# Kernel optimization log

Measured on AMD Instinct MI355X. Metric: run time of the kernel, lower is better.

The kernel has to match this reference:

```python
import jax, jax.numpy as jnp
import numpy as np

EMBED_DIM = 1024
NUM_HEADS = 16
HEAD_DIM = EMBED_DIM // NUM_HEADS


def setup_inputs() -> dict:
    key = jax.random.key(0)
    k1, k2, k3, k4 = jax.random.split(key, 4)
    S, B = 2048, 2
    x = jax.random.normal(k1, (S, B, EMBED_DIM), dtype=jnp.float32)
    # xavier_uniform for in_proj_weight [3E, E]
    limit_in = float(np.sqrt(6.0 / (3 * EMBED_DIM + EMBED_DIM)))
    in_proj_weight = jax.random.uniform(k2, (3 * EMBED_DIM, EMBED_DIM), minval=-limit_in, maxval=limit_in, dtype=jnp.float32)
    in_proj_bias = jnp.zeros((3 * EMBED_DIM,), dtype=jnp.float32)
    # out_proj: nn.Linear default init (kaiming-uniform-ish); use uniform of similar scale
    limit_out = float(np.sqrt(1.0 / EMBED_DIM))
    out_proj_weight = jax.random.uniform(k3, (EMBED_DIM, EMBED_DIM), minval=-limit_out, maxval=limit_out, dtype=jnp.float32)
    out_proj_bias = jnp.zeros((EMBED_DIM,), dtype=jnp.float32)
    return {
        "x": x,
        "in_proj_weight": in_proj_weight,
        "in_proj_bias": in_proj_bias,
        "out_proj_weight": out_proj_weight,
        "out_proj_bias": out_proj_bias,
    }


def reference(x, in_proj_weight, in_proj_bias, out_proj_weight, out_proj_bias):
    S, B, E = x.shape
    H, D = NUM_HEADS, HEAD_DIM
    scaling = float(D) ** -0.5
    # fused QKV projection: [S, B, 3E]
    qkv = jnp.einsum("sbe,fe->sbf", x, in_proj_weight) + in_proj_bias
    q, k, v = jnp.split(qkv, 3, axis=-1)
    q = q * scaling
    # [S, B, E] -> [B*H, S, D]
    def to_heads(t):
        return t.reshape(S, B * H, D).transpose(1, 0, 2)
    q, k, v = to_heads(q), to_heads(k), to_heads(v)
    # attention scores [B*H, S, S]
    scores = jnp.einsum("btd,bsd->bts", q, k)
    weights = jax.nn.softmax(scores, axis=-1)
    # dropout p=0.0 -> identity
    attn = jnp.einsum("bts,bsd->btd", weights, v)  # [B*H, S, D]
    attn = attn.transpose(1, 0, 2).reshape(S, B, E)
    out = jnp.einsum("sbe,fe->sbf", attn, out_proj_weight) + out_proj_bias
    return out
```

## Files before the change

### kernel.cpp

```cpp
#include <hip/hip_runtime.h>

typedef __bf16 bf16_t;
typedef __attribute__((ext_vector_type(8))) __bf16 bf16x8;
typedef __attribute__((ext_vector_type(4))) __bf16 bf16x4;
typedef __attribute__((ext_vector_type(4))) float f32x4;
typedef __attribute__((ext_vector_type(16))) float f32x16;

#define MFMA16(a, b, c) __builtin_amdgcn_mfma_f32_16x16x32_bf16((a), (b), (c), 0, 0, 0)
#define MFMA32(a, b, c) __builtin_amdgcn_mfma_f32_32x32x16_bf16((a), (b), (c), 0, 0, 0)
#define LOG2E 1.44269504088896f

__device__ __forceinline__ void async16(const bf16_t* g, bf16_t* l) {
    __builtin_amdgcn_global_load_lds(
        (const __attribute__((address_space(1))) unsigned int*)g,
        (__attribute__((address_space(3))) unsigned int*)l, 16, 0, 0);
}

__device__ __forceinline__ unsigned pack2(float a, float b) {
    union { bf16_t e[2]; unsigned u; } x;
    x.e[0] = (bf16_t)a; x.e[1] = (bf16_t)b;
    return x.u;
}

__global__ __launch_bounds__(256) void conv3(
    const float* __restrict__ s0, const float* __restrict__ s1,
    const float* __restrict__ s2, bf16_t* __restrict__ dst,
    int n0, int n1)
{
    const int i = (blockIdx.x * 256 + threadIdx.x) * 8;
    const float* src;
    int off;
    if (i < n0)           { src = s0; off = 0; }
    else if (i < n0 + n1) { src = s1; off = n0; }
    else                  { src = s2; off = n0 + n1; }
    const float4 a = *reinterpret_cast<const float4*>(src + i - off);
    const float4 b = *reinterpret_cast<const float4*>(src + i - off + 4);
    bf16x8 o;
    o[0] = (bf16_t)a.x; o[1] = (bf16_t)a.y; o[2] = (bf16_t)a.z; o[3] = (bf16_t)a.w;
    o[4] = (bf16_t)b.x; o[5] = (bf16_t)b.y; o[6] = (bf16_t)b.z; o[7] = (bf16_t)b.w;
    *reinterpret_cast<bf16x8*>(dst + i) = o;
}

__global__ __launch_bounds__(256) void vtrans(
    const bf16_t* __restrict__ qkv, bf16_t* __restrict__ vT, int B)
{
    const int bh = blockIdx.x, b = bh >> 4, h = bh & 15;
    const int s0 = blockIdx.y * 64;
    __shared__ bf16_t Ls[64][65];
    const int t = threadIdx.x;
    const int sl = t & 63, dc = t >> 6;
#pragma unroll
    for (int pass = 0; pass < 2; pass++) {
        const int d8 = dc + pass * 4;
        bf16x8 v = *reinterpret_cast<const bf16x8*>(
            qkv + (size_t)((s0 + sl) * B + b) * 3072 + 2048 + h * 64 + d8 * 8);
#pragma unroll
        for (int j = 0; j < 8; j++) Ls[sl][d8 * 8 + j] = v[j];
    }
    __syncthreads();
#pragma unroll
    for (int pass = 0; pass < 2; pass++) {
        const int cid = t + pass * 256;
        const int d = cid >> 3, cs = cid & 7;
        bf16x8 o;
#pragma unroll
        for (int j = 0; j < 8; j++) o[j] = Ls[cs * 8 + j][d];
        *reinterpret_cast<bf16x8*>(
            vT + (size_t)(bh * 64 + d) * 2048 + s0 + cs * 8) = o;
    }
}

template <int MT, bool F32OUT>
__global__ __launch_bounds__(256, 3) void gemm_nt_lds(
    const bf16_t* __restrict__ W, const bf16_t* __restrict__ X,
    const float* __restrict__ bias, void* __restrict__ Cv,
    int N, int K, int scale_lim, float qscale, int fpx)
{
    constexpr int NJ = MT / 32;
    __shared__ bf16_t As[2][128 * 32];
    __shared__ bf16_t Bs[2][MT * 32];

    const int lane = threadIdx.x & 63;
    const int wv   = threadIdx.x >> 6;
    const int l15  = lane & 15;
    const int qd   = lane >> 4;

    const int id = blockIdx.x;
    const int x8 = id & 7, k = id >> 3;
    const int fb = ((k % fpx) * 8 + x8) * 128;
    const int mb = (k / fpx) * MT;
    const int fw = (wv & 1) * 64;
    const int mw = (wv >> 1) * (MT / 2);

    f32x4 acc[4][NJ] = {};

    auto stage = [&](int set, int k0) {
#pragma unroll
        for (int t = 0; t < 2; t++) {
            const int p = (wv * 2 + t) * 64 + lane;
            const int r = p >> 2, cl = (p & 3) ^ (r & 3);
            async16(W + (size_t)(fb + r) * K + k0 + cl * 8,
                    &As[set][(wv * 2 + t) * 512]);
        }
#pragma unroll
        for (int t = 0; t < MT / 64; t++) {
            const int p = (wv * (MT / 64) + t) * 64 + lane;
            const int r = p >> 2, cl = (p & 3) ^ (r & 3);
            async16(X + (size_t)(mb + r) * K + k0 + cl * 8,
                    &Bs[set][(wv * (MT / 64) + t) * 512]);
        }
    };

    stage(0, 0);
    int set = 0;
    for (int k0 = 0; k0 < K; k0 += 32) {
        __syncthreads();
        if (k0 + 32 < K) stage(set ^ 1, k0 + 32);

        const int s3 = l15 & 3;
        bf16x8 a[4], bb[NJ];
#pragma unroll
        for (int i = 0; i < 4; i++)
            a[i] = *reinterpret_cast<const bf16x8*>(
                &As[set][(fw + i * 16 + l15) * 32 + ((qd ^ s3) * 8)]);
#pragma unroll
        for (int j = 0; j < NJ; j++)
            bb[j] = *reinterpret_cast<const bf16x8*>(
                &Bs[set][(mw + j * 16 + l15) * 32 + ((qd ^ s3) * 8)]);
#pragma unroll
        for (int i = 0; i < 4; i++)
#pragma unroll
            for (int j = 0; j < NJ; j++)
                acc[i][j] = MFMA16(a[i], bb[j], acc[i][j]);
        set ^= 1;
    }

    const float scale = (fb < scale_lim) ? qscale : 1.0f;
#pragma unroll
    for (int i = 0; i < 4; i++) {
        const int f0 = fb + fw + i * 16 + qd * 4;
        float bs[4];
#pragma unroll
        for (int r = 0; r < 4; r++) bs[r] = bias[f0 + r];
#pragma unroll
        for (int j = 0; j < NJ; j++) {
            const int m = mb + mw + j * 16 + l15;
            if (F32OUT) {
                float4 o;
                o.x = (acc[i][j][0] + bs[0]) * scale;
                o.y = (acc[i][j][1] + bs[1]) * scale;
                o.z = (acc[i][j][2] + bs[2]) * scale;
                o.w = (acc[i][j][3] + bs[3]) * scale;
                *reinterpret_cast<float4*>((float*)Cv + (size_t)m * N + f0) = o;
            } else {
                bf16x4 o;
#pragma unroll
                for (int r = 0; r < 4; r++)
                    o[r] = (bf16_t)((acc[i][j][r] + bs[r]) * scale);
                *reinterpret_cast<bf16x4*>((bf16_t*)Cv + (size_t)m * N + f0) = o;
            }
        }
    }
}

__global__ __launch_bounds__(256, 2) void flash_attn(
    const bf16_t* __restrict__ qkv, const bf16_t* __restrict__ vT,
    bf16_t* __restrict__ attn, int S, int B)
{
    const int E3 = 3072, E = 1024;
    const int bh = blockIdx.x, b = bh >> 4, h = bh & 15;
    const int tid = threadIdx.x, lane = tid & 63, wv = tid >> 6;
    const int qw = wv & 1;
    const int pr = wv >> 1;
    const int l31 = lane & 31, half = lane >> 5;

    __shared__ bf16_t Kt[2][2][64 * 64];
    __shared__ bf16_t Vt[2][2][64 * 64];
    __shared__ float  lsh[2][64];

    const int q0 = blockIdx.y * 128 + qw * 64;

    bf16x8 qf[2][4];
#pragma unroll
    for (int qt = 0; qt < 2; qt++) {
        const bf16_t* qp = qkv + (size_t)((q0 + qt * 32 + l31) * B + b) * E3 + h * 64;
#pragma unroll
        for (int ks = 0; ks < 4; ks++)
            qf[qt][ks] = *reinterpret_cast<const bf16x8*>(qp + ks * 16 + half * 8);
    }

    f32x16 oacc[2][2] = {};
    float lrun[2] = {0.0f, 0.0f};

    auto stage = [&](int set, int kv) {
#pragma unroll
        for (int t = 0; t < 4; t++) {
            const int p = (qw * 4 + t) * 64 + lane;
            const int r = p >> 3, cl = (p & 7) ^ (r & 7);
            async16(qkv + (size_t)((kv + r) * B + b) * E3 + E + h * 64 + cl * 8,
                    &Kt[pr][set][(qw * 4 + t) * 512]);
            async16(vT + (size_t)(bh * 64 + r) * 2048 + kv + cl * 8,
                    &Vt[pr][set][(qw * 4 + t) * 512]);
        }
    };

    const int kvbase = pr * (S / 2);
    const int NIT = S / 128;

    stage(0, kvbase);
    int set = 0;
    for (int it = 0; it < NIT; it++) {
        __syncthreads();
        if (it + 1 < NIT) stage(set ^ 1, kvbase + (it + 1) * 64);

        const bf16_t* K_ = Kt[pr][set];
        const bf16_t* V_ = Vt[pr][set];

        union PF { unsigned u[4]; bf16x8 v; };
        PF pf[2][4];
#pragma unroll
        for (int nt = 0; nt < 2; nt++) {
            const int r = nt * 32 + l31;
            const int r7 = r & 7;
            bf16x8 kf[4];
#pragma unroll
            for (int ks = 0; ks < 4; ks++)
                kf[ks] = *reinterpret_cast<const bf16x8*>(
                    K_ + r * 64 + (((ks * 2 + half) ^ r7) * 8));
#pragma unroll
            for (int qt = 0; qt < 2; qt++) {
                f32x16 st = {};
#pragma unroll
                for (int ks = 0; ks < 4; ks++)
                    st = MFMA32(kf[ks], qf[qt][ks], st);
                float ls = 0.0f;
                unsigned q8[8];
#pragma unroll
                for (int g = 0; g < 4; g++) {
                    const float p0 = __builtin_amdgcn_exp2f(st[4 * g]);
                    const float p1 = __builtin_amdgcn_exp2f(st[4 * g + 1]);
                    const float p2 = __builtin_amdgcn_exp2f(st[4 * g + 2]);
                    const float p3 = __builtin_amdgcn_exp2f(st[4 * g + 3]);
                    ls += (p0 + p1) + (p2 + p3);
                    q8[2 * g]     = pack2(p0, p1);
                    q8[2 * g + 1] = pack2(p2, p3);
                }
                lrun[qt] += ls;
                unsigned x8[8];
#pragma unroll
                for (int k = 0; k < 8; k++) x8[k] = __shfl_xor((int)q8[k], 32);
                pf[qt][nt * 2 + 0].u[0] = half ? x8[2] : q8[0];
                pf[qt][nt * 2 + 0].u[1] = half ? x8[3] : q8[1];
                pf[qt][nt * 2 + 0].u[2] = half ? q8[2] : x8[0];
                pf[qt][nt * 2 + 0].u[3] = half ? q8[3] : x8[1];
                pf[qt][nt * 2 + 1].u[0] = half ? x8[6] : q8[4];
                pf[qt][nt * 2 + 1].u[1] = half ? x8[7] : q8[5];
                pf[qt][nt * 2 + 1].u[2] = half ? q8[6] : x8[4];
                pf[qt][nt * 2 + 1].u[3] = half ? q8[7] : x8[5];
            }
        }
#pragma unroll
        for (int kn = 0; kn < 4; kn++)
#pragma unroll
            for (int dt = 0; dt < 2; dt++) {
                const int d = dt * 32 + l31;
                bf16x8 vf = *reinterpret_cast<const bf16x8*>(
                    V_ + d * 64 + (((kn * 2 + half) ^ (d & 7)) * 8));
                oacc[0][dt] = MFMA32(vf, pf[0][kn].v, oacc[0][dt]);
                oacc[1][dt] = MFMA32(vf, pf[1][kn].v, oacc[1][dt]);
            }
        set ^= 1;
    }

    __syncthreads();
    float lr[2];
#pragma unroll
    for (int qt = 0; qt < 2; qt++) lr[qt] = lrun[qt] + __shfl_xor(lrun[qt], 32);

    float* fo = reinterpret_cast<float*>(&Kt[0][0][0]) + qw * 4096;

    if (pr == 1) {
#pragma unroll
        for (int qt = 0; qt < 2; qt++) {
            const int ql = qt * 32 + l31;
            lsh[qw][ql] = lr[qt];
#pragma unroll
            for (int dt = 0; dt < 2; dt++)
#pragma unroll
                for (int g = 0; g < 4; g++)
#pragma unroll
                    for (int r = 0; r < 4; r++) {
                        const int d = dt * 32 + g * 8 + half * 4 + r;
                        fo[d * 64 + ql] = oacc[qt][dt][4 * g + r];
                    }
        }
    }
    __syncthreads();
    if (pr == 0) {
#pragma unroll
        for (int qt = 0; qt < 2; qt++) {
            const int ql = qt * 32 + l31;
            const float inv = 1.0f / (lr[qt] + lsh[qw][ql]);
            const int qrow = q0 + qt * 32 + l31;
#pragma unroll
            for (int dt = 0; dt < 2; dt++)
#pragma unroll
                for (int g = 0; g < 4; g++) {
                    bf16x4 o;
#pragma unroll
                    for (int r = 0; r < 4; r++) {
                        const int d = dt * 32 + g * 8 + half * 4 + r;
                        o[r] = (bf16_t)((oacc[qt][dt][4 * g + r] + fo[d * 64 + ql]) * inv);
                    }
                    *reinterpret_cast<bf16x4*>(attn + (size_t)(qrow * B + b) * E +
                                               h * 64 + dt * 32 + g * 8 + half * 4) = o;
                }
        }
    }
}

extern "C" void kernel_launch(void* const* d_in, const int* in_sizes, int n_in,
                              void* d_out, int out_size, void* d_ws, size_t ws_size,
                              hipStream_t stream) {
    const float* x  = (const float*)d_in[0];
    const float* wi = (const float*)d_in[1];
    const float* bi = (const float*)d_in[2];
    const float* wo = (const float*)d_in[3];
    const float* bo = (const float*)d_in[4];
    float* out = (float*)d_out;

    const int S = 2048, B = 2, E = 1024;
    const int M = S * B;

    bf16_t* xb   = (bf16_t*)d_ws;
    bf16_t* wib  = xb  + (size_t)M * E;
    bf16_t* wob  = wib + (size_t)3 * E * E;
    bf16_t* qkv  = wob + (size_t)E * E;
    bf16_t* attn = qkv + (size_t)M * 3 * E;
    bf16_t* vT   = xb;

    const int n0 = M * E, n1 = 3 * E * E, n2 = E * E;
    conv3<<<(n0 + n1 + n2) / 8 / 256, 256, 0, stream>>>(x, wi, wo, xb, n0, n1);

    gemm_nt_lds<128, false><<<(3 * E / 128) * (M / 128), 256, 0, stream>>>(
        wib, xb, bi, qkv, 3 * E, E, E, 0.125f * LOG2E, (3 * E / 128) / 8);

    vtrans<<<dim3(B * 16, S / 64), 256, 0, stream>>>(qkv, vT, B);

    flash_attn<<<dim3(B * 16, S / 128), 256, 0, stream>>>(qkv, vT, attn, S, B);

    gemm_nt_lds<64, true><<<(E / 128) * (M / 64), 256, 0, stream>>>(
        wob, attn, bo, out, E, E, 0, 1.0f, (E / 128) / 8);
}
```

Measured before the change: 198.4 us.

## Shrink flash-attention tiles to 32 queries per wave and 32-key steps

Each wave in the attention kernel now handles 32 query rows instead of 64, and each KV step is 32 keys instead of 64. K and V for a step share one smaller LDS buffer, and the V swizzle changes to match the narrower rows. The grid doubles along the query dimension and launch bounds rise to 4 blocks per CU, aiming for more occupancy and less register and LDS pressure. In exchange each K/V tile is reused by fewer queries, so there is more global and LDS traffic and twice as many loop iterations and barriers.

```diff
diff --git a/kernel.cpp b/kernel.cpp
--- a/kernel.cpp
+++ b/kernel.cpp
@@ -163,7 +163,7 @@
     }
 }
 
-__global__ __launch_bounds__(256, 2) void flash_attn(
+__global__ __launch_bounds__(256, 4) void flash_attn(
     const bf16_t* __restrict__ qkv, const bf16_t* __restrict__ vT,
     bf16_t* __restrict__ attn, int S, int B)
 {
@@ -174,148 +174,134 @@
     const int pr = wv >> 1;
     const int l31 = lane & 31, half = lane >> 5;
 
-    __shared__ bf16_t Kt[2][2][64 * 64];
-    __shared__ bf16_t Vt[2][2][64 * 64];
-    __shared__ float  lsh[2][64];
-
-    const int q0 = blockIdx.y * 128 + qw * 64;
-
-    bf16x8 qf[2][4];
-#pragma unroll
-    for (int qt = 0; qt < 2; qt++) {
-        const bf16_t* qp = qkv + (size_t)((q0 + qt * 32 + l31) * B + b) * E3 + h * 64;
+    __shared__ bf16_t KV[2][2][4096];
+    __shared__ float  lsh[2][32];
+
+    const int q0 = blockIdx.y * 64 + qw * 32;
+
+    bf16x8 qf[4];
+    {
+        const bf16_t* qp = qkv + (size_t)((q0 + l31) * B + b) * E3 + h * 64;
 #pragma unroll
         for (int ks = 0; ks < 4; ks++)
-            qf[qt][ks] = *reinterpret_cast<const bf16x8*>(qp + ks * 16 + half * 8);
-    }
-
-    f32x16 oacc[2][2] = {};
-    float lrun[2] = {0.0f, 0.0f};
+            qf[ks] = *reinterpret_cast<const bf16x8*>(qp + ks * 16 + half * 8);
+    }
+
+    f32x16 oacc[2] = {};
+    float lrun = 0.0f;
 
     auto stage = [&](int set, int kv) {
 #pragma unroll
-        for (int t = 0; t < 4; t++) {
-            const int p = (qw * 4 + t) * 64 + lane;
+        for (int t = 0; t < 2; t++) {
+            const int p = (qw * 2 + t) * 64 + lane;
             const int r = p >> 3, cl = (p & 7) ^ (r & 7);
             async16(qkv + (size_t)((kv + r) * B + b) * E3 + E + h * 64 + cl * 8,
-                    &Kt[pr][set][(qw * 4 + t) * 512]);
-            async16(vT + (size_t)(bh * 64 + r) * 2048 + kv + cl * 8,
-                    &Vt[pr][set][(qw * 4 + t) * 512]);
+                    &KV[pr][set][(qw * 2 + t) * 512]);
+        }
+#pragma unroll
+        for (int t = 0; t < 2; t++) {
+            const int p = (qw * 2 + t) * 64 + lane;
+            const int d = p >> 2, c = (p & 3) ^ (d & 3);
+            async16(vT + (size_t)(bh * 64 + d) * 2048 + kv + c * 8,
+                    &KV[pr][set][2048 + (qw * 2 + t) * 512]);
         }
     };
 
     const int kvbase = pr * (S / 2);
-    const int NIT = S / 128;
+    const int NIT = (S / 2) / 32;
 
     stage(0, kvbase);
     int set = 0;
     for (int it = 0; it < NIT; it++) {
         __syncthreads();
-        if (it + 1 < NIT) stage(set ^ 1, kvbase + (it + 1) * 64);
-
-        const bf16_t* K_ = Kt[pr][set];
-        const bf16_t* V_ = Vt[pr][set];
-
+        if (it + 1 < NIT) stage(set ^ 1, kvbase + (it + 1) * 32);
+
+        const bf16_t* K_ = KV[pr][set];
+        const bf16_t* V_ = KV[pr][set] + 2048;
+
+        f32x16 st = {};
+        const int r7 = l31 & 7;
+#pragma unroll
+        for (int ks = 0; ks < 4; ks++) {
+            bf16x8 kf = *reinterpret_cast<const bf16x8*>(
+                K_ + l31 * 64 + (((ks * 2 + half) ^ r7) * 8));
+            st = MFMA32(kf, qf[ks], st);
+        }
+
+        unsigned q8[8];
+        float ls = 0.0f;
+#pragma unroll
+        for (int g = 0; g < 4; g++) {
+            const float p0 = __builtin_amdgcn_exp2f(st[4 * g]);
+            const float p1 = __builtin_amdgcn_exp2f(st[4 * g + 1]);
+            const float p2 = __builtin_amdgcn_exp2f(st[4 * g + 2]);
+            const float p3 = __builtin_amdgcn_exp2f(st[4 * g + 3]);
+            ls += (p0 + p1) + (p2 + p3);
+            q8[2 * g]     = pack2(p0, p1);
+            q8[2 * g + 1] = pack2(p2, p3);
+        }
+        lrun += ls;
+
+        unsigned x8[8];
+#pragma unroll
+        for (int k = 0; k < 8; k++) x8[k] = __shfl_xor((int)q8[k], 32);
         union PF { unsigned u[4]; bf16x8 v; };
-        PF pf[2][4];
-#pragma unroll
-        for (int nt = 0; nt < 2; nt++) {
-            const int r = nt * 32 + l31;
-            const int r7 = r & 7;
-            bf16x8 kf[4];
-#pragma unroll
-            for (int ks = 0; ks < 4; ks++)
-                kf[ks] = *reinterpret_cast<const bf16x8*>(
-                    K_ + r * 64 + (((ks * 2 + half) ^ r7) * 8));
-#pragma unroll
-            for (int qt = 0; qt < 2; qt++) {
-                f32x16 st = {};
-#pragma unroll
-                for (int ks = 0; ks < 4; ks++)
-                    st = MFMA32(kf[ks], qf[qt][ks], st);
-                float ls = 0.0f;
-                unsigned q8[8];
-#pragma unroll
-                for (int g = 0; g < 4; g++) {
-                    const float p0 = __builtin_amdgcn_exp2f(st[4 * g]);
-                    const float p1 = __builtin_amdgcn_exp2f(st[4 * g + 1]);
-                    const float p2 = __builtin_amdgcn_exp2f(st[4 * g + 2]);
-                    const float p3 = __builtin_amdgcn_exp2f(st[4 * g + 3]);
-                    ls += (p0 + p1) + (p2 + p3);
-                    q8[2 * g]     = pack2(p0, p1);
-                    q8[2 * g + 1] = pack2(p2, p3);
-                }
-                lrun[qt] += ls;
-                unsigned x8[8];
-#pragma unroll
-                for (int k = 0; k < 8; k++) x8[k] = __shfl_xor((int)q8[k], 32);
-                pf[qt][nt * 2 + 0].u[0] = half ? x8[2] : q8[0];
-                pf[qt][nt * 2 + 0].u[1] = half ? x8[3] : q8[1];
-                pf[qt][nt * 2 + 0].u[2] = half ? q8[2] : x8[0];
-                pf[qt][nt * 2 + 0].u[3] = half ? q8[3] : x8[1];
-                pf[qt][nt * 2 + 1].u[0] = half ? x8[6] : q8[4];
-                pf[qt][nt * 2 + 1].u[1] = half ? x8[7] : q8[5];
-                pf[qt][nt * 2 + 1].u[2] = half ? q8[6] : x8[4];
-                pf[qt][nt * 2 + 1].u[3] = half ? q8[7] : x8[5];
-            }
-        }
-#pragma unroll
-        for (int kn = 0; kn < 4; kn++)
+        PF pf[2];
+        pf[0].u[0] = half ? x8[2] : q8[0];
+        pf[0].u[1] = half ? x8[3] : q8[1];
+        pf[0].u[2] = half ? q8[2] : x8[0];
+        pf[0].u[3] = half ? q8[3] : x8[1];
+        pf[1].u[0] = half ? x8[6] : q8[4];
+        pf[1].u[1] = half ? x8[7] : q8[5];
+        pf[1].u[2] = half ? q8[6] : x8[4];
+        pf[1].u[3] = half ? q8[7] : x8[5];
+
+#pragma unroll
+        for (int kn = 0; kn < 2; kn++)
 #pragma unroll
             for (int dt = 0; dt < 2; dt++) {
                 const int d = dt * 32 + l31;
                 bf16x8 vf = *reinterpret_cast<const bf16x8*>(
-                    V_ + d * 64 + (((kn * 2 + half) ^ (d & 7)) * 8));
-                oacc[0][dt] = MFMA32(vf, pf[0][kn].v, oacc[0][dt]);
-                oacc[1][dt] = MFMA32(vf, pf[1][kn].v, oacc[1][dt]);
+                    V_ + d * 32 + (((kn * 2 + half) ^ (d & 3)) * 8));
+                oacc[dt] = MFMA32(vf, pf[kn].v, oacc[dt]);
             }
         set ^= 1;
     }
 
     __syncthreads();
-    float lr[2];
-#pragma unroll
-    for (int qt = 0; qt < 2; qt++) lr[qt] = lrun[qt] + __shfl_xor(lrun[qt], 32);
-
-    float* fo = reinterpret_cast<float*>(&Kt[0][0][0]) + qw * 4096;
+    const float lr = lrun + __shfl_xor(lrun, 32);
+
+    float* fo = reinterpret_cast<float*>(&KV[0][0][0]) + qw * 2048;
 
     if (pr == 1) {
-#pragma unroll
-        for (int qt = 0; qt < 2; qt++) {
-            const int ql = qt * 32 + l31;
-            lsh[qw][ql] = lr[qt];
-#pragma unroll
-            for (int dt = 0; dt < 2; dt++)
-#pragma unroll
-                for (int g = 0; g < 4; g++)
-#pragma unroll
-                    for (int r = 0; r < 4; r++) {
-                        const int d = dt * 32 + g * 8 + half * 4 + r;
-                        fo[d * 64 + ql] = oacc[qt][dt][4 * g + r];
-                    }
-        }
+        lsh[qw][l31] = lr;
+#pragma unroll
+        for (int dt = 0; dt < 2; dt++)
+#pragma unroll
+            for (int g = 0; g < 4; g++)
+#pragma unroll
+                for (int r = 0; r < 4; r++) {
+                    const int d = dt * 32 + g * 8 + half * 4 + r;
+                    fo[d * 32 + l31] = oacc[dt][4 * g + r];
+                }
     }
     __syncthreads();
     if (pr == 0) {
-#pragma unroll
-        for (int qt = 0; qt < 2; qt++) {
-            const int ql = qt * 32 + l31;
-            const float inv = 1.0f / (lr[qt] + lsh[qw][ql]);
-            const int qrow = q0 + qt * 32 + l31;
-#pragma unroll
-            for (int dt = 0; dt < 2; dt++)
-#pragma unroll
-                for (int g = 0; g < 4; g++) {
-                    bf16x4 o;
-#pragma unroll
-                    for (int r = 0; r < 4; r++) {
-                        const int d = dt * 32 + g * 8 + half * 4 + r;
-                        o[r] = (bf16_t)((oacc[qt][dt][4 * g + r] + fo[d * 64 + ql]) * inv);
-                    }
-                    *reinterpret_cast<bf16x4*>(attn + (size_t)(qrow * B + b) * E +
-                                               h * 64 + dt * 32 + g * 8 + half * 4) = o;
+        const float inv = 1.0f / (lr + lsh[qw][l31]);
+        const int qrow = q0 + l31;
+#pragma unroll
+        for (int dt = 0; dt < 2; dt++)
+#pragma unroll
+            for (int g = 0; g < 4; g++) {
+                bf16x4 o;
+#pragma unroll
+                for (int r = 0; r < 4; r++) {
+                    const int d = dt * 32 + g * 8 + half * 4 + r;
+                    o[r] = (bf16_t)((oacc[dt][4 * g + r] + fo[d * 32 + l31]) * inv);
                 }
-        }
+                *reinterpret_cast<bf16x4*>(attn + (size_t)(qrow * B + b) * E +
+                                           h * 64 + dt * 32 + g * 8 + half * 4) = o;
+            }
     }
 }
 
@@ -347,7 +333,7 @@
 
     vtrans<<<dim3(B * 16, S / 64), 256, 0, stream>>>(qkv, vT, B);
 
-    flash_attn<<<dim3(B * 16, S / 128), 256, 0, stream>>>(qkv, vT, attn, S, B);
+    flash_attn<<<dim3(B * 16, S / 64), 256, 0, stream>>>(qkv, vT, attn, S, B);
 
     gemm_nt_lds<64, true><<<(E / 128) * (M / 64), 256, 0, stream>>>(
         wob, attn, bo, out, E, E, 0, 1.0f, (E / 128) / 8);
```

Result: slower. 210.0 us (+5.9%).
